# Performance work log

Hardware: AMD Instinct MI355X
Metric: run time of the kernel (lower is better)

## Reference

```python
import jax, jax.numpy as jnp
import numpy as np

B, N, T1, T2, K = 16, 2048, 12, 64, 3


def setup_inputs() -> dict:
    key = jax.random.key(0)
    ks = jax.random.split(key, 16)
    g = lambda k, s, sc=1.0: jax.random.normal(k, s, dtype=jnp.float32) * sc
    X = g(ks[0], (B, N, 1, T1))
    A = jax.random.uniform(ks[1], (N, N), dtype=jnp.float32)
    Vs = g(ks[2], (N, N), 1.0 / np.sqrt(N))
    bs = g(ks[3], (N, N), 0.01)
    W1 = jax.random.uniform(ks[4], (T1,), dtype=jnp.float32)
    W2 = g(ks[5], (1, T1), 1.0)
    W3 = jax.random.uniform(ks[6], (1,), dtype=jnp.float32)
    Ve = g(ks[7], (T1, T1), 1.0 / np.sqrt(T1))
    be = g(ks[8], (T1, T1), 0.01)
    U1 = jax.random.uniform(ks[9], (N,), dtype=jnp.float32) / np.sqrt(N)
    U2 = g(ks[10], (1, N), 1.0 / np.sqrt(N))
    U3 = jax.random.uniform(ks[11], (1,), dtype=jnp.float32)
    Wcheb = g(ks[12], (K, T1, T2), 1.0 / np.sqrt(T1))
    bcheb = jnp.zeros((T2,), jnp.float32)
    return dict(X=X, A=A, Vs=Vs, bs=bs, W1=W1, W2=W2, W3=W3, Ve=Ve, be=be,
                U1=U1, U2=U2, U3=U3, Wcheb=Wcheb, bcheb=bcheb)


def reference(X, A, Vs, bs, W1, W2, W3, Ve, be, U1, U2, U3, Wcheb, bcheb):
    # ---- SpatialAtt (C=1). NOTE: faithful to source, the resulting A_hat = A*S
    # is computed in the torch forward but NEVER used downstream (gcn params are
    # built from plain A). jit will DCE this branch.
    W1x = jnp.einsum('bnct,t->bnc', X, W1)            # [B,N,1]
    W3x = jnp.einsum('c,bnct->bnt', W3, X)            # [B,N,T1]
    Ssc = jnp.einsum('bnt,bmt->bnm', jnp.einsum('bnc,ct->bnt', W1x, W2), W3x) + bs
    S = jax.nn.softmax(jnp.einsum('nm,bml->bnl', Vs, jax.nn.softmax(Ssc, axis=1)), axis=1)
    _A_hat = A[None] * S  # unused (matches source)

    # ---- TemporalAtt
    xT = jnp.transpose(X, (0, 3, 2, 1))               # [B,T1,1,N]
    E1 = jnp.einsum('btc,cn->btn', jnp.einsum('btcn,n->btc', xT, U1), U2)  # [B,T1,N]
    U3x = jnp.einsum('c,bnct->bnt', U3, X)            # [B,N,T1]
    Esc = jnp.einsum('btn,bns->bts', E1, U3x) + be    # [B,T1,T1]
    E = jax.nn.softmax(jnp.einsum('ts,bsu->btu', Ve, jax.nn.softmax(Esc, axis=1)), axis=1)

    # E.repeat(1,N,1).view(B,N,T,T) broadcasts the same [T,T] per node
    x2 = X[:, :, 0, :]                                # [B,N,T1]
    X_hat = jnp.einsum('bnt,btu->bnu', x2, E)         # [B,N,T1]

    # ---- ChebConv, sym normalization, lambda_max = 2 -> L_hat = -D^{-1/2} A D^{-1/2}
    # deg from row-sums (scatter over edge_index[0]); aggregation at target (col),
    # so applying L_hat is a transpose-matmul in dense form.
    deg = A.sum(axis=1)
    dis = jnp.where(deg > 0, jax.lax.rsqrt(jnp.where(deg > 0, deg, 1.0)), 0.0)
    M = -(dis[:, None] * A * dis[None, :])            # [N,N]
    Lx = lambda h: jnp.einsum('rc,brt->bct', M, h)    # out[col] += norm * x[row]

    Tx_prev = X_hat
    out = jnp.einsum('bnt,to->bno', X_hat, Wcheb[0])
    Tx = Lx(X_hat)
    if K > 1:
        out = out + jnp.einsum('bnt,to->bno', Tx, Wcheb[1])
    for k in range(2, K):
        Tx_new = 2.0 * Lx(Tx) - Tx_prev
        out = out + jnp.einsum('bnt,to->bno', Tx_new, Wcheb[k])
        Tx_prev, Tx = Tx, Tx_new
    out = jax.nn.relu(out + bcheb)
    return out.reshape(B, N, 1, T2)
```

## Files before the change

kernel.cpp:

```cpp
#include <hip/hip_runtime.h>
#include <math.h>

#define NN 2048
#define BB 16
#define T1D 12
#define T2D 64
#define JJ (BB*T1D)

typedef short short8 __attribute__((ext_vector_type(8)));
typedef float f32x4 __attribute__((ext_vector_type(4)));

#define OFF_DIS   0
#define OFF_E     2048
#define OFF_XH    4352
#define OFF_P1    (OFF_XH + NN*JJ)
#define OFF_P2    (OFF_P1 + NN*JJ)
#define OFF_XHBT  (OFF_P2 + NN*JJ)
#define OFF_P1BT  (OFF_XHBT + NN*JJ/2)
#define OFF_ABT   (OFF_P1BT + NN*JJ/2)
#define OFF_PPART (OFF_ABT + NN*NN/2)

__device__ inline ushort f2bf(float f) {
    union { float f; unsigned int u; } x; x.f = f;
    unsigned int u = x.u + 0x7fffu + ((x.u >> 16) & 1u);
    return (ushort)(u >> 16);
}

__global__ __launch_bounds__(256) void k_deg(const float* __restrict__ A,
                                             float* __restrict__ dis) {
    int wid = threadIdx.x >> 6, lane = threadIdx.x & 63;
    int r = blockIdx.x * 4 + wid;
    const float4* Ar = (const float4*)(A + (size_t)r * NN);
    float s = 0.f;
#pragma unroll
    for (int i = 0; i < 8; ++i) {
        float4 v = Ar[i * 64 + lane];
        s += v.x + v.y + v.z + v.w;
    }
#pragma unroll
    for (int off = 32; off > 0; off >>= 1) s += __shfl_down(s, off);
    if (lane == 0) dis[r] = (s > 0.f) ? rsqrtf(s) : 0.f;
}

__global__ __launch_bounds__(256) void k_conv(const float* __restrict__ A,
                                              const float* __restrict__ dis,
                                              ushort* __restrict__ AbT) {
    __shared__ float lds[64][65];
    int t = threadIdx.x;
    int c0 = blockIdx.x * 64, k0 = blockIdx.y * 64;
#pragma unroll
    for (int i = 0; i < 4; ++i) {
        int idx = t + i * 256;
        int kr = idx >> 4, c4 = idx & 15;
        float4 v = *(const float4*)&A[(size_t)(k0 + kr) * NN + c0 + c4 * 4];
        float dk = dis[k0 + kr];
        lds[c4 * 4 + 0][kr] = v.x * dk;
        lds[c4 * 4 + 1][kr] = v.y * dk;
        lds[c4 * 4 + 2][kr] = v.z * dk;
        lds[c4 * 4 + 3][kr] = v.w * dk;
    }
    __syncthreads();
    int cl = t >> 2, ck = (t & 3) * 16;
    float dc = dis[c0 + cl];
    union { ushort us[8]; uint4 v; } p0, p1;
#pragma unroll
    for (int e = 0; e < 8; ++e) p0.us[e] = f2bf(lds[cl][ck + e] * dc);
#pragma unroll
    for (int e = 0; e < 8; ++e) p1.us[e] = f2bf(lds[cl][ck + 8 + e] * dc);
    *(uint4*)&AbT[(size_t)(c0 + cl) * NN + k0 + ck] = p0.v;
    *(uint4*)&AbT[(size_t)(c0 + cl) * NN + k0 + ck + 8] = p1.v;
}

__global__ __launch_bounds__(256) void k_prepE(const float* __restrict__ X,
                                               const float* __restrict__ U1,
                                               const float* __restrict__ U2,
                                               const float* __restrict__ U3,
                                               const float* __restrict__ be,
                                               const float* __restrict__ Ve,
                                               float* __restrict__ E_ws) {
    int b = blockIdx.x, tid = threadIdx.x;
    __shared__ float red[24][256];
    __shared__ float es[T1D][T1D];

    float accr[T1D], accc[T1D];
#pragma unroll
    for (int t = 0; t < T1D; ++t) { accr[t] = 0.f; accc[t] = 0.f; }

    for (int n = tid; n < NN; n += 256) {
        const float* xp = X + ((size_t)b * NN + n) * T1D;
        float x[T1D];
        *(float4*)&x[0] = *(const float4*)&xp[0];
        *(float4*)&x[4] = *(const float4*)&xp[4];
        *(float4*)&x[8] = *(const float4*)&xp[8];
        float u1 = U1[n], u2 = U2[n];
#pragma unroll
        for (int t = 0; t < T1D; ++t) {
            accr[t] += x[t] * u1;
            accc[t] += x[t] * u2;
        }
    }
#pragma unroll
    for (int t = 0; t < T1D; ++t) {
        red[t][tid] = accr[t];
        red[12 + t][tid] = accc[t];
    }
    __syncthreads();
    for (int s = 128; s > 0; s >>= 1) {
        if (tid < s) {
#pragma unroll
            for (int a = 0; a < 24; ++a) red[a][tid] += red[a][tid + s];
        }
        __syncthreads();
    }

    float u3 = U3[0];
    if (tid < T1D) {
        int s = tid;
        float cs = red[12 + s][0] * u3;
        float vals[T1D];
        float m = -1e30f;
#pragma unroll
        for (int t = 0; t < T1D; ++t) {
            vals[t] = red[t][0] * cs + be[t * T1D + s];
            m = fmaxf(m, vals[t]);
        }
        float sum = 0.f;
#pragma unroll
        for (int t = 0; t < T1D; ++t) { vals[t] = expf(vals[t] - m); sum += vals[t]; }
        float inv = 1.f / sum;
#pragma unroll
        for (int t = 0; t < T1D; ++t) es[t][s] = vals[t] * inv;
    }
    __syncthreads();
    if (tid < T1D) {
        int u = tid;
        float vals[T1D];
        float m = -1e30f;
#pragma unroll
        for (int t = 0; t < T1D; ++t) {
            float acc = 0.f;
#pragma unroll
            for (int s = 0; s < T1D; ++s) acc += Ve[t * T1D + s] * es[s][u];
            vals[t] = acc;
            m = fmaxf(m, acc);
        }
        float sum = 0.f;
#pragma unroll
        for (int t = 0; t < T1D; ++t) { vals[t] = expf(vals[t] - m); sum += vals[t]; }
        float inv = 1.f / sum;
#pragma unroll
        for (int t = 0; t < T1D; ++t) E_ws[b * 144 + t * T1D + u] = vals[t] * inv;
    }
}

__global__ __launch_bounds__(256) void k_xhat(const float* __restrict__ X,
                                              const float* __restrict__ E_ws,
                                              float* __restrict__ Xh) {
    int g = blockIdx.x * 256 + threadIdx.x;
    int n = g / JJ;
    int j = g - n * JJ;
    int b = j / T1D;
    int u = j - b * T1D;
    const float* xp = X + ((size_t)b * NN + n) * T1D;
    const float* ep = E_ws + b * 144 + u;
    float acc = 0.f;
#pragma unroll
    for (int t = 0; t < T1D; ++t) acc += xp[t] * ep[t * T1D];
    Xh[g] = acc;
}

__global__ __launch_bounds__(256) void k_redt(const float* __restrict__ parts,
                                              int SP,
                                              float* __restrict__ out32,
                                              ushort* __restrict__ outbt) {
    __shared__ float lds[16][193];
    int t = threadIdx.x;
    int c0 = blockIdx.x * 16;
    const float4* base = (const float4*)parts + (size_t)c0 * 48;
#pragma unroll
    for (int i = 0; i < 3; ++i) {
        int idx = t + i * 256;
        float4 s = base[idx];
        for (int p = 1; p < SP; ++p) {
            float4 v = base[(size_t)p * (NN * JJ / 4) + idx];
            s.x += v.x; s.y += v.y; s.z += v.z; s.w += v.w;
        }
        int row = idx / 48, c4 = idx % 48;
        *(float4*)&out32[(size_t)(c0 + row) * JJ + c4 * 4] = s;
        lds[row][c4 * 4 + 0] = s.x;
        lds[row][c4 * 4 + 1] = s.y;
        lds[row][c4 * 4 + 2] = s.z;
        lds[row][c4 * 4 + 3] = s.w;
    }
    __syncthreads();
    if (t < JJ) {
        union { ushort us[8]; uint4 v; } p0, p1;
#pragma unroll
        for (int n = 0; n < 8; ++n) p0.us[n] = f2bf(lds[n][t]);
#pragma unroll
        for (int n = 0; n < 8; ++n) p1.us[n] = f2bf(lds[8 + n][t]);
        *(uint4*)&outbt[(size_t)t * NN + c0] = p0.v;
        *(uint4*)&outbt[(size_t)t * NN + c0 + 8] = p1.v;
    }
}

__global__ __launch_bounds__(256) void k_red2(const float* __restrict__ parts,
                                              int SP,
                                              float* __restrict__ out32) {
    int g = blockIdx.x * 256 + threadIdx.x;
    const float4* base = (const float4*)parts;
    float4 s = base[g];
    for (int p = 1; p < SP; ++p) {
        float4 v = base[(size_t)p * (NN * JJ / 4) + g];
        s.x += v.x; s.y += v.y; s.z += v.z; s.w += v.w;
    }
    ((float4*)out32)[g] = s;
}

__global__ __launch_bounds__(256) void k_gemm(const ushort* __restrict__ AbT,
                                              const ushort* __restrict__ Zbt,
                                              float* __restrict__ Ppart,
                                              int Ksplit, int nch) {
    int tid = threadIdx.x;
    int wave = tid >> 6, lane = tid & 63;
    int jl = lane & 15;
    int kl = (lane >> 4) * 8;
    int c0 = blockIdx.x * 64 + wave * 16;
    int kbase = blockIdx.y * Ksplit + kl;

    const ushort* arow = AbT + (size_t)(c0 + jl) * NN;
    f32x4 acc[12];
#pragma unroll
    for (int n = 0; n < 12; ++n) acc[n] = (f32x4)0.f;

    for (int ch = 0; ch < nch; ++ch) {
        int koff = kbase + ch * 32;
        short8 bfr[12];
#pragma unroll
        for (int n = 0; n < 12; ++n)
            bfr[n] = *(const short8*)&Zbt[(size_t)(n * 16 + jl) * NN + koff];
        short8 a = *(const short8*)&arow[koff];
#pragma unroll
        for (int n = 0; n < 12; ++n)
            acc[n] = __builtin_amdgcn_mfma_f32_16x16x32_bf16(a, bfr[n], acc[n], 0, 0, 0);
    }

    float* Pp = Ppart + (size_t)blockIdx.y * (NN * JJ);
    int crow = c0 + (lane >> 4) * 4;
#pragma unroll
    for (int n = 0; n < 12; ++n) {
#pragma unroll
        for (int r = 0; r < 4; ++r)
            Pp[(size_t)(crow + r) * JJ + n * 16 + jl] = acc[n][r];
    }
}

__global__ __launch_bounds__(256) void k_out(const float* __restrict__ Xh,
                                             const float* __restrict__ P1,
                                             const float* __restrict__ P2,
                                             const float* __restrict__ Wcheb,
                                             const float* __restrict__ bcheb,
                                             float* __restrict__ out) {
    int g = blockIdx.x * 256 + threadIdx.x;
    int o = g & 63;
    int row = g >> 6;
    int b = row >> 11;
    int n = row & 2047;
    int base = n * JJ + b * T1D;
    const float* xh = Xh + base;
    const float* p1 = P1 + base;
    const float* p2 = P2 + base;
    const float* W0 = Wcheb;
    const float* W1 = Wcheb + 768;
    const float* W2 = Wcheb + 1536;
    float acc = bcheb[o];
#pragma unroll
    for (int t = 0; t < T1D; ++t) {
        float w0 = W0[t * 64 + o], w1 = W1[t * 64 + o], w2 = W2[t * 64 + o];
        acc += xh[t] * (w0 - w2) - p1[t] * w1 + 2.f * p2[t] * w2;
    }
    out[g] = fmaxf(acc, 0.f);
}

extern "C" void kernel_launch(void* const* d_in, const int* in_sizes, int n_in,
                              void* d_out, int out_size, void* d_ws, size_t ws_size,
                              hipStream_t stream) {
    const float* X  = (const float*)d_in[0];
    const float* A  = (const float*)d_in[1];
    const float* Ve = (const float*)d_in[7];
    const float* be = (const float*)d_in[8];
    const float* U1 = (const float*)d_in[9];
    const float* U2 = (const float*)d_in[10];
    const float* U3 = (const float*)d_in[11];
    const float* Wc = (const float*)d_in[12];
    const float* bc = (const float*)d_in[13];
    float* out = (float*)d_out;

    float* w     = (float*)d_ws;
    float* dis   = w + OFF_DIS;
    float* E     = w + OFF_E;
    float* Xh    = w + OFF_XH;
    float* P1    = w + OFF_P1;
    float* P2    = w + OFF_P2;
    ushort* Xhbt = (ushort*)(w + OFF_XHBT);
    ushort* P1bt = (ushort*)(w + OFF_P1BT);
    ushort* AbT  = (ushort*)(w + OFF_ABT);
    float* Ppart = w + OFF_PPART;

    int SP = 8;
    while (SP > 1 && ((size_t)OFF_PPART + (size_t)SP * NN * JJ) * 4 > ws_size) SP >>= 1;
    int Ksplit = NN / SP;
    int nch = Ksplit / 32;

    k_deg<<<NN / 4, 256, 0, stream>>>(A, dis);
    k_conv<<<dim3(32, 32), 256, 0, stream>>>(A, dis, AbT);
    k_prepE<<<BB, 256, 0, stream>>>(X, U1, U2, U3, be, Ve, E);
    k_xhat<<<(NN * JJ) / 256, 256, 0, stream>>>(X, E, Xh);
    k_redt<<<NN / 16, 256, 0, stream>>>(Xh, 1, Xh, Xhbt);
    k_gemm<<<dim3(NN / 64, SP), 256, 0, stream>>>(AbT, Xhbt, Ppart, Ksplit, nch);
    k_redt<<<NN / 16, 256, 0, stream>>>(Ppart, SP, P1, P1bt);
    k_gemm<<<dim3(NN / 64, SP), 256, 0, stream>>>(AbT, P1bt, Ppart, Ksplit, nch);
    k_red2<<<(NN * JJ / 4) / 256, 256, 0, stream>>>(Ppart, SP, P2);
    k_out<<<(BB * NN * T2D) / 256, 256, 0, stream>>>(Xh, P1, P2, Wc, bc, out);
}
```

Measured before the change: 195.4 us.

## Fuse prep kernels and do in-block split-K reduction in GEMM

Merges the degree and temporal-attention kernels into one launch, and merges the A conversion with X_hat computation and bf16 transpose into one launch. The GEMM is restructured so each block's 8 waves split K over the full 2048 and reduce the partial sums through LDS, writing P and its bf16 transpose directly. This removes the global split-K partial buffers and the separate reduction kernels, cutting launches and memory traffic. In exchange each block does less work per output tile and adds an LDS reduction plus scattered transposed bf16 stores.

```diff
diff --git a/kernel.cpp b/kernel.cpp
--- a/kernel.cpp
+++ b/kernel.cpp
@@ -5,20 +5,19 @@
 #define BB 16
 #define T1D 12
 #define T2D 64
-#define JJ (BB*T1D)
+#define JJ 192
 
 typedef short short8 __attribute__((ext_vector_type(8)));
 typedef float f32x4 __attribute__((ext_vector_type(4)));
 
 #define OFF_DIS   0
 #define OFF_E     2048
-#define OFF_XH    4352
+#define OFF_XH    4608
 #define OFF_P1    (OFF_XH + NN*JJ)
 #define OFF_P2    (OFF_P1 + NN*JJ)
 #define OFF_XHBT  (OFF_P2 + NN*JJ)
 #define OFF_P1BT  (OFF_XHBT + NN*JJ/2)
 #define OFF_ABT   (OFF_P1BT + NN*JJ/2)
-#define OFF_PPART (OFF_ABT + NN*NN/2)
 
 __device__ inline ushort f2bf(float f) {
     union { float f; unsigned int u; } x; x.f = f;
@@ -26,66 +25,39 @@
     return (ushort)(u >> 16);
 }
 
-__global__ __launch_bounds__(256) void k_deg(const float* __restrict__ A,
-                                             float* __restrict__ dis) {
-    int wid = threadIdx.x >> 6, lane = threadIdx.x & 63;
-    int r = blockIdx.x * 4 + wid;
-    const float4* Ar = (const float4*)(A + (size_t)r * NN);
-    float s = 0.f;
-#pragma unroll
-    for (int i = 0; i < 8; ++i) {
-        float4 v = Ar[i * 64 + lane];
-        s += v.x + v.y + v.z + v.w;
-    }
-#pragma unroll
-    for (int off = 32; off > 0; off >>= 1) s += __shfl_down(s, off);
-    if (lane == 0) dis[r] = (s > 0.f) ? rsqrtf(s) : 0.f;
-}
-
-__global__ __launch_bounds__(256) void k_conv(const float* __restrict__ A,
-                                              const float* __restrict__ dis,
-                                              ushort* __restrict__ AbT) {
-    __shared__ float lds[64][65];
-    int t = threadIdx.x;
-    int c0 = blockIdx.x * 64, k0 = blockIdx.y * 64;
-#pragma unroll
-    for (int i = 0; i < 4; ++i) {
-        int idx = t + i * 256;
-        int kr = idx >> 4, c4 = idx & 15;
-        float4 v = *(const float4*)&A[(size_t)(k0 + kr) * NN + c0 + c4 * 4];
-        float dk = dis[k0 + kr];
-        lds[c4 * 4 + 0][kr] = v.x * dk;
-        lds[c4 * 4 + 1][kr] = v.y * dk;
-        lds[c4 * 4 + 2][kr] = v.z * dk;
-        lds[c4 * 4 + 3][kr] = v.w * dk;
-    }
-    __syncthreads();
-    int cl = t >> 2, ck = (t & 3) * 16;
-    float dc = dis[c0 + cl];
-    union { ushort us[8]; uint4 v; } p0, p1;
-#pragma unroll
-    for (int e = 0; e < 8; ++e) p0.us[e] = f2bf(lds[cl][ck + e] * dc);
-#pragma unroll
-    for (int e = 0; e < 8; ++e) p1.us[e] = f2bf(lds[cl][ck + 8 + e] * dc);
-    *(uint4*)&AbT[(size_t)(c0 + cl) * NN + k0 + ck] = p0.v;
-    *(uint4*)&AbT[(size_t)(c0 + cl) * NN + k0 + ck + 8] = p1.v;
-}
-
-__global__ __launch_bounds__(256) void k_prepE(const float* __restrict__ X,
-                                               const float* __restrict__ U1,
-                                               const float* __restrict__ U2,
-                                               const float* __restrict__ U3,
-                                               const float* __restrict__ be,
-                                               const float* __restrict__ Ve,
-                                               float* __restrict__ E_ws) {
-    int b = blockIdx.x, tid = threadIdx.x;
+__global__ __launch_bounds__(256) void k_degE(const float* __restrict__ A,
+                                              const float* __restrict__ X,
+                                              const float* __restrict__ U1,
+                                              const float* __restrict__ U2,
+                                              const float* __restrict__ U3,
+                                              const float* __restrict__ be,
+                                              const float* __restrict__ Ve,
+                                              float* __restrict__ dis,
+                                              float* __restrict__ E_ws) {
     __shared__ float red[24][256];
     __shared__ float es[T1D][T1D];
-
+    int tid = threadIdx.x;
+
+    if (blockIdx.x < 512) {
+        int wid = tid >> 6, lane = tid & 63;
+        int r = blockIdx.x * 4 + wid;
+        const float4* Ar = (const float4*)(A + (size_t)r * NN);
+        float s = 0.f;
+#pragma unroll
+        for (int i = 0; i < 8; ++i) {
+            float4 v = Ar[i * 64 + lane];
+            s += v.x + v.y + v.z + v.w;
+        }
+#pragma unroll
+        for (int off = 32; off > 0; off >>= 1) s += __shfl_down(s, off);
+        if (lane == 0) dis[r] = (s > 0.f) ? rsqrtf(s) : 0.f;
+        return;
+    }
+
+    int b = blockIdx.x - 512;
     float accr[T1D], accc[T1D];
 #pragma unroll
     for (int t = 0; t < T1D; ++t) { accr[t] = 0.f; accc[t] = 0.f; }
-
     for (int n = tid; n < NN; n += 256) {
         const float* xp = X + ((size_t)b * NN + n) * T1D;
         float x[T1D];
@@ -112,7 +84,6 @@
         }
         __syncthreads();
     }
-
     float u3 = U3[0];
     if (tid < T1D) {
         int s = tid;
@@ -153,105 +124,133 @@
     }
 }
 
-__global__ __launch_bounds__(256) void k_xhat(const float* __restrict__ X,
-                                              const float* __restrict__ E_ws,
-                                              float* __restrict__ Xh) {
-    int g = blockIdx.x * 256 + threadIdx.x;
-    int n = g / JJ;
-    int j = g - n * JJ;
-    int b = j / T1D;
-    int u = j - b * T1D;
-    const float* xp = X + ((size_t)b * NN + n) * T1D;
-    const float* ep = E_ws + b * 144 + u;
-    float acc = 0.f;
-#pragma unroll
-    for (int t = 0; t < T1D; ++t) acc += xp[t] * ep[t * T1D];
-    Xh[g] = acc;
-}
-
-__global__ __launch_bounds__(256) void k_redt(const float* __restrict__ parts,
-                                              int SP,
-                                              float* __restrict__ out32,
-                                              ushort* __restrict__ outbt) {
-    __shared__ float lds[16][193];
+__global__ __launch_bounds__(256) void k_mid(const float* __restrict__ A,
+                                             const float* __restrict__ dis,
+                                             const float* __restrict__ X,
+                                             const float* __restrict__ E_ws,
+                                             ushort* __restrict__ AbT,
+                                             float* __restrict__ Xh,
+                                             ushort* __restrict__ Xhbt) {
+    __shared__ float lds[5504];
     int t = threadIdx.x;
-    int c0 = blockIdx.x * 16;
-    const float4* base = (const float4*)parts + (size_t)c0 * 48;
+
+    if (blockIdx.x < 1024) {
+        int c0 = (blockIdx.x & 31) * 64, k0 = (blockIdx.x >> 5) * 64;
+#pragma unroll
+        for (int i = 0; i < 4; ++i) {
+            int idx = t + i * 256;
+            int kr = idx >> 4, c4 = idx & 15;
+            float4 v = *(const float4*)&A[(size_t)(k0 + kr) * NN + c0 + c4 * 4];
+            float dk = dis[k0 + kr];
+            lds[(c4 * 4 + 0) * 65 + kr] = v.x * dk;
+            lds[(c4 * 4 + 1) * 65 + kr] = v.y * dk;
+            lds[(c4 * 4 + 2) * 65 + kr] = v.z * dk;
+            lds[(c4 * 4 + 3) * 65 + kr] = v.w * dk;
+        }
+        __syncthreads();
+        int cl = t >> 2, ck = (t & 3) * 16;
+        float dc = dis[c0 + cl];
+        union { ushort us[8]; uint4 v; } p0, p1;
+#pragma unroll
+        for (int e = 0; e < 8; ++e) p0.us[e] = f2bf(lds[cl * 65 + ck + e] * dc);
+#pragma unroll
+        for (int e = 0; e < 8; ++e) p1.us[e] = f2bf(lds[cl * 65 + ck + 8 + e] * dc);
+        *(uint4*)&AbT[(size_t)(c0 + cl) * NN + k0 + ck] = p0.v;
+        *(uint4*)&AbT[(size_t)(c0 + cl) * NN + k0 + ck + 8] = p1.v;
+        return;
+    }
+
+    int n0 = (blockIdx.x - 1024) * 16;
+    float* EL = lds + 3200;
+#pragma unroll
+    for (int i = 0; i < 9; ++i) {
+        int idx = t + i * 256;
+        if (idx < 2304) EL[idx] = E_ws[idx];
+    }
+    __syncthreads();
+    {
+        int nr = t >> 4, b = t & 15;
+        const float* xp = X + ((size_t)b * NN + n0 + nr) * T1D;
+        float x[T1D];
+        *(float4*)&x[0] = *(const float4*)&xp[0];
+        *(float4*)&x[4] = *(const float4*)&xp[4];
+        *(float4*)&x[8] = *(const float4*)&xp[8];
+        const float* Eb = EL + b * 144;
+#pragma unroll
+        for (int u = 0; u < T1D; ++u) {
+            float acc = 0.f;
+#pragma unroll
+            for (int tt = 0; tt < T1D; ++tt) acc += x[tt] * Eb[tt * T1D + u];
+            lds[nr * 200 + b * T1D + u] = acc;
+        }
+    }
+    __syncthreads();
 #pragma unroll
     for (int i = 0; i < 3; ++i) {
-        int idx = t + i * 256;
-        float4 s = base[idx];
-        for (int p = 1; p < SP; ++p) {
-            float4 v = base[(size_t)p * (NN * JJ / 4) + idx];
-            s.x += v.x; s.y += v.y; s.z += v.z; s.w += v.w;
-        }
-        int row = idx / 48, c4 = idx % 48;
-        *(float4*)&out32[(size_t)(c0 + row) * JJ + c4 * 4] = s;
-        lds[row][c4 * 4 + 0] = s.x;
-        lds[row][c4 * 4 + 1] = s.y;
-        lds[row][c4 * 4 + 2] = s.z;
-        lds[row][c4 * 4 + 3] = s.w;
-    }
-    __syncthreads();
+        int idx4 = t + i * 256;
+        int row = idx4 / 48, c4 = idx4 % 48;
+        *(float4*)&Xh[(size_t)(n0 + row) * JJ + c4 * 4] =
+            *(float4*)&lds[row * 200 + c4 * 4];
+    }
     if (t < JJ) {
         union { ushort us[8]; uint4 v; } p0, p1;
 #pragma unroll
-        for (int n = 0; n < 8; ++n) p0.us[n] = f2bf(lds[n][t]);
-#pragma unroll
-        for (int n = 0; n < 8; ++n) p1.us[n] = f2bf(lds[8 + n][t]);
-        *(uint4*)&outbt[(size_t)t * NN + c0] = p0.v;
-        *(uint4*)&outbt[(size_t)t * NN + c0 + 8] = p1.v;
-    }
-}
-
-__global__ __launch_bounds__(256) void k_red2(const float* __restrict__ parts,
-                                              int SP,
-                                              float* __restrict__ out32) {
-    int g = blockIdx.x * 256 + threadIdx.x;
-    const float4* base = (const float4*)parts;
-    float4 s = base[g];
-    for (int p = 1; p < SP; ++p) {
-        float4 v = base[(size_t)p * (NN * JJ / 4) + g];
-        s.x += v.x; s.y += v.y; s.z += v.z; s.w += v.w;
-    }
-    ((float4*)out32)[g] = s;
-}
-
-__global__ __launch_bounds__(256) void k_gemm(const ushort* __restrict__ AbT,
+        for (int nr = 0; nr < 8; ++nr) p0.us[nr] = f2bf(lds[nr * 200 + t]);
+#pragma unroll
+        for (int nr = 0; nr < 8; ++nr) p1.us[nr] = f2bf(lds[(8 + nr) * 200 + t]);
+        *(uint4*)&Xhbt[(size_t)t * NN + n0] = p0.v;
+        *(uint4*)&Xhbt[(size_t)t * NN + n0 + 8] = p1.v;
+    }
+}
+
+template<int NFRAG, bool WBT>
+__global__ __launch_bounds__(512) void k_gemm(const ushort* __restrict__ AbT,
                                               const ushort* __restrict__ Zbt,
-                                              float* __restrict__ Ppart,
-                                              int Ksplit, int nch) {
+                                              float* __restrict__ P,
+                                              ushort* __restrict__ Pbt) {
+    __shared__ float lds[8 * NFRAG * 64 * 4];
     int tid = threadIdx.x;
     int wave = tid >> 6, lane = tid & 63;
     int jl = lane & 15;
     int kl = (lane >> 4) * 8;
-    int c0 = blockIdx.x * 64 + wave * 16;
-    int kbase = blockIdx.y * Ksplit + kl;
-
-    const ushort* arow = AbT + (size_t)(c0 + jl) * NN;
-    f32x4 acc[12];
-#pragma unroll
-    for (int n = 0; n < 12; ++n) acc[n] = (f32x4)0.f;
-
-    for (int ch = 0; ch < nch; ++ch) {
-        int koff = kbase + ch * 32;
-        short8 bfr[12];
-#pragma unroll
-        for (int n = 0; n < 12; ++n)
-            bfr[n] = *(const short8*)&Zbt[(size_t)(n * 16 + jl) * NN + koff];
+    int c0 = blockIdx.x * 16;
+    int j0 = blockIdx.y * (16 * NFRAG);
+    int kbase = wave * 256 + kl;
+
+    const ushort* arow = AbT + (size_t)(c0 + jl) * NN + kbase;
+    f32x4 acc[NFRAG];
+#pragma unroll
+    for (int n = 0; n < NFRAG; ++n) acc[n] = (f32x4)0.f;
+
+#pragma unroll
+    for (int ch = 0; ch < 8; ++ch) {
+        int koff = ch * 32;
         short8 a = *(const short8*)&arow[koff];
-#pragma unroll
-        for (int n = 0; n < 12; ++n)
+        short8 bfr[NFRAG];
+#pragma unroll
+        for (int n = 0; n < NFRAG; ++n)
+            bfr[n] = *(const short8*)&Zbt[(size_t)(j0 + n * 16 + jl) * NN + kbase + koff];
+#pragma unroll
+        for (int n = 0; n < NFRAG; ++n)
             acc[n] = __builtin_amdgcn_mfma_f32_16x16x32_bf16(a, bfr[n], acc[n], 0, 0, 0);
     }
 
-    float* Pp = Ppart + (size_t)blockIdx.y * (NN * JJ);
-    int crow = c0 + (lane >> 4) * 4;
-#pragma unroll
-    for (int n = 0; n < 12; ++n) {
-#pragma unroll
-        for (int r = 0; r < 4; ++r)
-            Pp[(size_t)(crow + r) * JJ + n * 16 + jl] = acc[n][r];
+#pragma unroll
+    for (int n = 0; n < NFRAG; ++n)
+        *(f32x4*)&lds[((wave * NFRAG + n) * 64 + lane) * 4] = acc[n];
+    __syncthreads();
+
+    const int NOUT = 16 * 16 * NFRAG;
+    for (int o = tid; o < NOUT; o += 512) {
+        int c_idx = o / (16 * NFRAG);
+        int j_idx = o % (16 * NFRAG);
+        int n = j_idx >> 4, col = j_idx & 15;
+        int lidx = ((c_idx >> 2) * 16 + col) * 4 + (c_idx & 3);
+        float s = 0.f;
+#pragma unroll
+        for (int w = 0; w < 8; ++w) s += lds[(w * NFRAG + n) * 256 + lidx];
+        P[(size_t)(c0 + c_idx) * JJ + j0 + j_idx] = s;
+        if (WBT) Pbt[(size_t)(j0 + j_idx) * NN + c0 + c_idx] = f2bf(s);
     }
 }
 
@@ -305,21 +304,10 @@
     ushort* Xhbt = (ushort*)(w + OFF_XHBT);
     ushort* P1bt = (ushort*)(w + OFF_P1BT);
     ushort* AbT  = (ushort*)(w + OFF_ABT);
-    float* Ppart = w + OFF_PPART;
-
-    int SP = 8;
-    while (SP > 1 && ((size_t)OFF_PPART + (size_t)SP * NN * JJ) * 4 > ws_size) SP >>= 1;
-    int Ksplit = NN / SP;
-    int nch = Ksplit / 32;
-
-    k_deg<<<NN / 4, 256, 0, stream>>>(A, dis);
-    k_conv<<<dim3(32, 32), 256, 0, stream>>>(A, dis, AbT);
-    k_prepE<<<BB, 256, 0, stream>>>(X, U1, U2, U3, be, Ve, E);
-    k_xhat<<<(NN * JJ) / 256, 256, 0, stream>>>(X, E, Xh);
-    k_redt<<<NN / 16, 256, 0, stream>>>(Xh, 1, Xh, Xhbt);
-    k_gemm<<<dim3(NN / 64, SP), 256, 0, stream>>>(AbT, Xhbt, Ppart, Ksplit, nch);
-    k_redt<<<NN / 16, 256, 0, stream>>>(Ppart, SP, P1, P1bt);
-    k_gemm<<<dim3(NN / 64, SP), 256, 0, stream>>>(AbT, P1bt, Ppart, Ksplit, nch);
-    k_red2<<<(NN * JJ / 4) / 256, 256, 0, stream>>>(Ppart, SP, P2);
+
+    k_degE<<<528, 256, 0, stream>>>(A, X, U1, U2, U3, be, Ve, dis, E);
+    k_mid<<<1152, 256, 0, stream>>>(A, dis, X, E, AbT, Xh, Xhbt);
+    k_gemm<3, true ><<<dim3(128, 4), 512, 0, stream>>>(AbT, Xhbt, P1, P1bt);
+    k_gemm<3, false><<<dim3(128, 4), 512, 0, stream>>>(AbT, P1bt, P2, nullptr);
     k_out<<<(BB * NN * T2D) / 256, 256, 0, stream>>>(Xh, P1, P2, Wc, bc, out);
 }
```

After: 180.6 us. -7.6%, faster.
